# Performance work log

Measured on AMD Instinct MI355X. Metric: run time of the kernel, lower is better.

Reference implementation:

```python
import jax, jax.numpy as jnp
import numpy as np

B, N, C, H, W = 4, 5, 64, 96, 288
DOWNSAMPLE_RATE = 4
DISCRETE_RATIO = 0.4
DECAY_WEIGHTS = jax.nn.softmax(jnp.array([1.0, 0.5], dtype=jnp.float32))  # frame=1, decay=0.5


def _warp_one(img, theta):
    # img: (C,H,W), theta: (2,3). Matches F.affine_grid + F.grid_sample
    # (bilinear, zeros padding, align_corners=True).
    c, h, w = img.shape
    xs = jnp.linspace(-1.0, 1.0, w, dtype=img.dtype)
    ys = jnp.linspace(-1.0, 1.0, h, dtype=img.dtype)
    gy, gx = jnp.meshgrid(ys, xs, indexing='ij')
    base = jnp.stack([gx.ravel(), gy.ravel(), jnp.ones(h * w, img.dtype)], 0)  # (3, HW)
    g = theta @ base  # (2, HW) normalized coords
    px = (g[0] + 1.0) * 0.5 * (w - 1)
    py = (g[1] + 1.0) * 0.5 * (h - 1)
    x0 = jnp.floor(px); y0 = jnp.floor(py)
    wx = px - x0; wy = py - y0
    def tap(yy, xx):
        yi = jnp.clip(yy, 0, h - 1).astype(jnp.int32)
        xi = jnp.clip(xx, 0, w - 1).astype(jnp.int32)
        valid = ((yy >= 0) & (yy <= h - 1) & (xx >= 0) & (xx <= w - 1)).astype(img.dtype)
        return img[:, yi, xi] * valid  # (C, HW)
    out = (tap(y0, x0) * (1 - wx) * (1 - wy)
           + tap(y0, x0 + 1) * wx * (1 - wy)
           + tap(y0 + 1, x0) * (1 - wx) * wy
           + tap(y0 + 1, x0 + 1) * wx * wy)
    return out.reshape(c, h, w)


def _frame_score(hist, mlp_w, mlp_b):
    # hist: (B,N,C,H,W) -> per-pixel ego-vs-neighbor attention score (B,N,1,H,W).
    b, n, c, h, w = hist.shape
    node = hist.reshape(b, n, c, h * w).transpose(0, 3, 1, 2)  # (B, P, N, C)
    ego = node[:, :, 0]          # (B, P, C)
    neigh = node[:, :, 1:]       # (B, P, N-1, C)
    # Query rows are all the repeated ego vector -> one row suffices (identical math).
    s = jnp.einsum('bpc,bpkc->bpk', ego, neigh) / jnp.sqrt(jnp.asarray(c, hist.dtype))
    attn = jax.nn.softmax(s, axis=-1)
    ctx = jnp.einsum('bpk,bpkc->bpc', attn, neigh)
    sc = jax.nn.sigmoid(ctx @ mlp_w.T + mlp_b)                   # (B, P, 1)
    sc = jnp.broadcast_to(sc[:, :, None, :], (b, h * w, n - 1, 1))
    ego_sc = jnp.ones((b, h * w, 1, 1), hist.dtype)
    overall = jnp.concatenate([ego_sc, sc], axis=2)              # (B, P, N, 1)
    return overall.transpose(0, 2, 3, 1).reshape(b, n, 1, h, w)


def _forward(x0, x1, pairwise_t_matrix, mlp_w, mlp_b):
    x0g = x0.reshape(B, N, C, H, W)
    x1g = x1.reshape(B, N, C, H, W)

    # --- TemporalSampling: weighted per-frame scores, threshold, 3x3 max-pool ---
    conf = DECAY_WEIGHTS[0] * _frame_score(x0g, mlp_w, mlp_b) \
         + DECAY_WEIGHTS[1] * _frame_score(x1g, mlp_w, mlp_b)      # (B,N,1,H,W)
    mask = jnp.where(conf > 0.5, jnp.float32(1.0), jnp.float32(0.0))
    mask = jax.lax.reduce_window(mask, -jnp.inf, jax.lax.max,
                                 (1, 1, 1, 3, 3), (1, 1, 1, 1, 1), 'SAME')
    x = x0g * mask  # broadcast over C

    # --- normalize pairwise transform to 2x3 affine matrices ---
    t = pairwise_t_matrix[:, :, :, jnp.array([0, 1])][:, :, :, :, jnp.array([0, 1, 3])]  # (B,L,L,2,3)
    t = t.at[..., 0, 1].mul(H / W)
    t = t.at[..., 1, 0].mul(W / H)
    t = t.at[..., 0, 2].set(t[..., 0, 2] / (DOWNSAMPLE_RATE * DISCRETE_RATIO * W) * 2)
    t = t.at[..., 1, 2].set(t[..., 1, 2] / (DOWNSAMPLE_RATE * DISCRETE_RATIO * H) * 2)
    theta = t[:, 0]  # (B,N,2,3): warp each cav into ego frame

    # --- per-agent warp ---
    warped = jax.vmap(jax.vmap(_warp_one))(x, theta)  # (B,N,C,H,W)

    # --- AttenFusion: per-pixel NxN attention, keep ego row ---
    nf = warped.reshape(B, N, C, H * W).transpose(0, 3, 1, 2)  # (B, P, N, C)
    s = jnp.einsum('bpc,bpkc->bpk', nf[:, :, 0], nf) / jnp.sqrt(jnp.asarray(C, nf.dtype))
    attn = jax.nn.softmax(s, axis=-1)
    ctx = jnp.einsum('bpk,bpkc->bpc', attn, nf)                 # (B, P, C)
    x_fuse = ctx.transpose(0, 2, 1).reshape(B, C, H, W)
    return x_fuse


def setup_inputs() -> dict:
    key = jax.random.key(0)
    k0, k1, k2, k3 = jax.random.split(key, 4)
    x0 = jax.random.normal(k0, (B * N, C, H, W), dtype=jnp.float32)
    x1 = jax.random.normal(k1, (B * N, C, H, W), dtype=jnp.float32)
    eye = jnp.broadcast_to(jnp.eye(4, dtype=jnp.float32), (B, N, N, 4, 4))
    pairwise_t_matrix = eye + 0.01 * jax.random.normal(k2, (B, N, N, 4, 4), dtype=jnp.float32)
    mlp_w = 0.1 * jax.random.normal(k3, (1, C), dtype=jnp.float32)
    mlp_b = jnp.zeros((1,), dtype=jnp.float32)
    record_len = jnp.full((B,), N, dtype=jnp.int32)
    return {"x0": x0, "x1": x1, "pairwise_t_matrix": pairwise_t_matrix,
            "mlp_w": mlp_w, "mlp_b": mlp_b, "record_len": record_len}


def reference(x0, x1, pairwise_t_matrix, mlp_w, mlp_b, record_len):
    # record_len is uniform (=N) and only determines the static regrouping.
    return _forward(x0, x1, pairwise_t_matrix, mlp_w, mlp_b)
```

## Files before the change

### kernel.cpp

```cpp
#include <hip/hip_runtime.h>
#include <cmath>

#define BB 4
#define NN 5
#define CC 64
#define HH 96
#define WW 288
#define PP (HH*WW)
#define QP (PP/4)
#define BP (BB*PP)
#define BQ (BP/4)
#define TPITCH 65


static __device__ __forceinline__ float sigmoidf_(float x) {
    return 1.0f / (1.0f + expf(-x));
}
static __device__ __forceinline__ float4 f4zero() {
    return make_float4(0.f, 0.f, 0.f, 0.f);
}
static __device__ __forceinline__ void fma4s(float4& a, float s, const float4& v) {
    a.x += s * v.x; a.y += s * v.y; a.z += s * v.z; a.w += s * v.w;
}
static __device__ __forceinline__ void fma44(float4& a, const float4& s, const float4& v) {
    a.x += s.x * v.x; a.y += s.y * v.y; a.z += s.z * v.z; a.w += s.w * v.w;
}
static __device__ __forceinline__ float dot4(const float4& a, const float4& b) {
    return a.x*b.x + a.y*b.y + a.z*b.z + a.w*b.w;
}
static __device__ __forceinline__ float score4(const float* dd, const float* mm, float bias) {
    float s0 = dd[0]*0.125f, s1 = dd[1]*0.125f, s2 = dd[2]*0.125f, s3 = dd[3]*0.125f;
    float mx = fmaxf(fmaxf(s0, s1), fmaxf(s2, s3));
    float e0 = expf(s0-mx), e1 = expf(s1-mx), e2 = expf(s2-mx), e3 = expf(s3-mx);
    float inv = 1.0f / (e0+e1+e2+e3);
    float z = (e0*mm[0] + e1*mm[1] + e2*mm[2] + e3*mm[3]) * inv + bias;
    return sigmoidf_(z);
}

static __device__ __forceinline__ void theta_load(
    const float* __restrict__ pmat, int b, int n,
    float& t00, float& t01, float& t02, float& t10, float& t11, float& t12)
{
    const float* m = pmat + ((size_t)(b * NN + 0) * NN + n) * 16;
    t00 = m[0];
    t01 = m[1] * ((float)HH / (float)WW);
    t02 = m[3] * (float)(2.0 / (4.0 * 0.4 * (double)WW));
    t10 = m[4] * ((float)WW / (float)HH);
    t11 = m[5];
    t12 = m[7] * (float)(2.0 / (4.0 * 0.4 * (double)HH));
}

__global__ __launch_bounds__(256) void x1_part_kernel(
    const float4* __restrict__ x1, const float* __restrict__ mlp_w,
    float4* __restrict__ dpart1)
{
    int q   = blockIdx.x * 256 + threadIdx.x;
    int seg = blockIdx.y;
    int b  = q / QP;
    int qp = q - b * QP;
    const float4* base = x1 + (size_t)b * (NN*CC*QP) + qp;

    float4 d[4] = {f4zero(), f4zero(), f4zero(), f4zero()};
    float4 m[4] = {f4zero(), f4zero(), f4zero(), f4zero()};
    #pragma unroll 4
    for (int ci = 0; ci < 16; ci++) {
        int c = seg * 16 + ci;
        float4 e  = base[(size_t)c * QP];
        float  wc = mlp_w[c];
        #pragma unroll
        for (int k = 1; k < NN; k++) {
            float4 v = base[((size_t)k * CC + c) * QP];
            fma44(d[k-1], e, v);
            fma4s(m[k-1], wc, v);
        }
    }
    #pragma unroll
    for (int j = 0; j < 4; j++) {
        dpart1[((size_t)seg * 8 + j)     * BQ + q] = d[j];
        dpart1[((size_t)seg * 8 + 4 + j) * BQ + q] = m[j];
    }
}

__global__ __launch_bounds__(256) void transpose_mask_kernel(
    const float4* __restrict__ x0f4, const float* __restrict__ mlp_w,
    float4* __restrict__ x0t, float* __restrict__ dpx0)
{
    __shared__ float A[64 * TPITCH];
    __shared__ float Bsh[64 * TPITCH];
    __shared__ float redD[256];
    __shared__ float redM[256];
    __shared__ float wlds[64];

    int t   = threadIdx.x;
    int b   = blockIdx.y;
    int pt0 = blockIdx.x * 64;
    int c   = t >> 2, pq = t & 3;
    int pix = t >> 2, cg = t & 3;

    if (t < 64) wlds[t] = mlp_w[t];

    {
        const float4* src = x0f4 + ((size_t)(b*NN + 0) * CC + c) * QP
                                 + blockIdx.x * 16 + pq * 4;
        float4 r[4];
        #pragma unroll
        for (int j = 0; j < 4; j++) r[j] = src[j];
        #pragma unroll
        for (int j = 0; j < 4; j++) {
            int col = pq * 16 + j * 4;
            A[c*TPITCH + col+0] = r[j].x;
            A[c*TPITCH + col+1] = r[j].y;
            A[c*TPITCH + col+2] = r[j].z;
            A[c*TPITCH + col+3] = r[j].w;
        }
    }
    __syncthreads();
    float a[16];
    {
        #pragma unroll
        for (int j = 0; j < 16; j++) a[j] = A[(cg*16 + j)*TPITCH + pix];
        float4* dst = x0t + ((size_t)(b*NN + 0) * PP + pt0 + pix) * 16 + cg * 4;
        #pragma unroll
        for (int jj = 0; jj < 4; jj++)
            dst[jj] = make_float4(a[jj*4+0], a[jj*4+1], a[jj*4+2], a[jj*4+3]);
    }

    for (int k = 1; k < NN; k++) {
        const float4* src = x0f4 + ((size_t)(b*NN + k) * CC + c) * QP
                                 + blockIdx.x * 16 + pq * 4;
        float4 r[4];
        #pragma unroll
        for (int j = 0; j < 4; j++) r[j] = src[j];
        __syncthreads();
        #pragma unroll
        for (int j = 0; j < 4; j++) {
            int col = pq * 16 + j * 4;
            Bsh[c*TPITCH + col+0] = r[j].x;
            Bsh[c*TPITCH + col+1] = r[j].y;
            Bsh[c*TPITCH + col+2] = r[j].z;
            Bsh[c*TPITCH + col+3] = r[j].w;
        }
        __syncthreads();
        float bv[16];
        #pragma unroll
        for (int j = 0; j < 16; j++) bv[j] = Bsh[(cg*16 + j)*TPITCH + pix];
        float4* dst = x0t + ((size_t)(b*NN + k) * PP + pt0 + pix) * 16 + cg * 4;
        #pragma unroll
        for (int jj = 0; jj < 4; jj++)
            dst[jj] = make_float4(bv[jj*4+0], bv[jj*4+1], bv[jj*4+2], bv[jj*4+3]);

        float sd = 0.f, sm = 0.f;
        #pragma unroll
        for (int j = 0; j < 16; j++) {
            sd += a[j] * bv[j];
            sm += wlds[cg*16 + j] * bv[j];
        }
        redD[t] = sd;
        redM[t] = sm;
        __syncthreads();
        if (t < 64) {
            float dd = redD[t*4] + redD[t*4+1] + redD[t*4+2] + redD[t*4+3];
            float mm = redM[t*4] + redM[t*4+1] + redM[t*4+2] + redM[t*4+3];
            int gp = b * PP + pt0 + t;
            dpx0[(size_t)(k-1)   * BP + gp] = dd;
            dpx0[(size_t)(4+k-1) * BP + gp] = mm;
        }
    }
}

__global__ __launch_bounds__(256) void comb_kernel(
    const float4* __restrict__ dpart1, const float4* __restrict__ dpx0,
    const float* __restrict__ mlp_b, float4* __restrict__ premask)
{
    int q = blockIdx.x * 256 + threadIdx.x;
    float bias = mlp_b[0];

    float4 d1[8];
    #pragma unroll
    for (int j = 0; j < 8; j++) {
        float4 s = f4zero();
        #pragma unroll
        for (int seg = 0; seg < 4; seg++) {
            float4 v = dpart1[((size_t)seg * 8 + j) * BQ + q];
            s.x += v.x; s.y += v.y; s.z += v.z; s.w += v.w;
        }
        d1[j] = s;
    }
    float4 d0[8];
    #pragma unroll
    for (int j = 0; j < 8; j++) d0[j] = dpx0[(size_t)j * BQ + q];

    const float W0 = 0.6224593312018546f, W1 = 0.3775406687981454f;
    float4 res;
    #pragma unroll
    for (int kcomp = 0; kcomp < 4; kcomp++) {
        float dd0[4], mm0[4], dd1[4], mm1[4];
        #pragma unroll
        for (int j = 0; j < 4; j++) {
            dd0[j] = ((const float*)&d0[j])[kcomp];
            mm0[j] = ((const float*)&d0[4+j])[kcomp];
            dd1[j] = ((const float*)&d1[j])[kcomp];
            mm1[j] = ((const float*)&d1[4+j])[kcomp];
        }
        float sc0 = score4(dd0, mm0, bias);
        float sc1 = score4(dd1, mm1, bias);
        float conf = W0 * sc0 + W1 * sc1;
        ((float*)&res)[kcomp] = (conf > 0.5f) ? 1.f : 0.f;
    }
    premask[q] = res;
}

__global__ __launch_bounds__(256) void pool_kernel(
    const float* __restrict__ pre, float4* __restrict__ pooled)
{
    int q  = blockIdx.x * 256 + threadIdx.x;
    int b  = q / QP;
    int qp = q - b * QP;
    int p0 = qp * 4;
    int h  = p0 / WW;
    int w0 = p0 - h * WW;
    const float* pb = pre + (size_t)b * PP;
    float m[4] = {0.f, 0.f, 0.f, 0.f};
    #pragma unroll
    for (int dy = -1; dy <= 1; dy++) {
        int y = h + dy;
        if (y < 0 || y >= HH) continue;
        const float* row = pb + y * WW;
        float c_[6];
        float4 mid = *(const float4*)(row + w0);
        c_[0] = (w0 > 0) ? row[w0 - 1] : 0.f;
        c_[1] = mid.x; c_[2] = mid.y; c_[3] = mid.z; c_[4] = mid.w;
        c_[5] = (w0 + 4 < WW) ? row[w0 + 4] : 0.f;
        #pragma unroll
        for (int j = 0; j < 4; j++)
            m[j] = fmaxf(m[j], fmaxf(c_[j], fmaxf(c_[j+1], c_[j+2])));
    }
    pooled[q] = make_float4(m[0], m[1], m[2], m[3]);
}

__global__ __launch_bounds__(256) void fuse_kernel(
    const float4* __restrict__ x0t, const float* __restrict__ pmat,
    const float* __restrict__ pooled, float* __restrict__ out)
{
    int g   = blockIdx.x * 256 + threadIdx.x;
    int pix = g >> 4;
    int cq  = g & 15;
    int b = pix / PP;
    int p = pix - b * PP;
    int h = p / WW;
    int w = p - h * WW;

    float gx = -1.0f + 2.0f * (float)w / (float)(WW - 1);
    float gy = -1.0f + 2.0f * (float)h / (float)(HH - 1);
    const float* poolb = pooled + (size_t)b * PP;

    float4 wv[NN];
    #pragma unroll
    for (int n = 0; n < NN; n++) {
        float t00, t01, t02, t10, t11, t12;
        theta_load(pmat, b, n, t00, t01, t02, t10, t11, t12);
        float g0 = t00 * gx + t01 * gy + t02;
        float g1 = t10 * gx + t11 * gy + t12;
        float fx = (g0 + 1.0f) * 0.5f * (float)(WW - 1);
        float fy = (g1 + 1.0f) * 0.5f * (float)(HH - 1);
        float x0f = floorf(fx), y0f = floorf(fy);
        float wx = fx - x0f, wy = fy - y0f;
        float bw[4] = { (1.f - wx) * (1.f - wy), wx * (1.f - wy),
                        (1.f - wx) * wy,         wx * wy };
        const float4* fr = x0t + (size_t)(b * NN + n) * PP * 16;
        float4 acc = f4zero();
        #pragma unroll
        for (int t = 0; t < 4; t++) {
            float xx = (t & 1) ? (x0f + 1.0f) : x0f;
            float yy = (t >> 1) ? (y0f + 1.0f) : y0f;
            int xi = min(max((int)xx, 0), WW - 1);
            int yi = min(max((int)yy, 0), HH - 1);
            float valid = (yy >= 0.0f && yy <= (float)(HH - 1) &&
                           xx >= 0.0f && xx <= (float)(WW - 1)) ? 1.0f : 0.0f;
            int off = yi * WW + xi;
            float mk = (n == 0) ? 1.0f : poolb[off];
            float wgt = bw[t] * valid * mk;
            float4 v = fr[(size_t)off * 16 + cq];
            fma4s(acc, wgt, v);
        }
        wv[n] = acc;
    }

    float dt[NN];
    #pragma unroll
    for (int n = 0; n < NN; n++) dt[n] = dot4(wv[0], wv[n]);
    #pragma unroll
    for (int n = 0; n < NN; n++) {
        #pragma unroll
        for (int msk = 1; msk < 16; msk <<= 1)
            dt[n] += __shfl_xor(dt[n], msk, 16);
    }

    float s[NN], attn[NN];
    float mx = -INFINITY;
    #pragma unroll
    for (int n = 0; n < NN; n++) { s[n] = dt[n] * 0.125f; mx = fmaxf(mx, s[n]); }
    float sum = 0.f;
    #pragma unroll
    for (int n = 0; n < NN; n++) { attn[n] = expf(s[n] - mx); sum += attn[n]; }
    float inv = 1.0f / sum;

    float4 o = f4zero();
    #pragma unroll
    for (int n = 0; n < NN; n++) fma4s(o, attn[n] * inv, wv[n]);

    size_t ob = ((size_t)(b * CC + cq * 4)) * PP + p;
    out[ob]                = o.x;
    out[ob + (size_t)PP]   = o.y;
    out[ob + (size_t)2*PP] = o.z;
    out[ob + (size_t)3*PP] = o.w;
}

extern "C" void kernel_launch(void* const* d_in, const int* in_sizes, int n_in,
                              void* d_out, int out_size, void* d_ws, size_t ws_size,
                              hipStream_t stream) {
    float*       x0    = (float*)d_in[0];
    float*       x1    = (float*)d_in[1];
    const float* pmat  = (const float*)d_in[2];
    const float* mlp_w = (const float*)d_in[3];
    const float* mlp_b = (const float*)d_in[4];
    float* out = (float*)d_out;

    float4* x0f4    = (float4*)x0;
    float4* x1f4    = (float4*)x1;
    float4* out4    = (float4*)out;
    float4* dpart1  = out4;
    float*  dpx0_f  = out + (size_t)128 * BQ;
    float4* dpx0_4  = (float4*)dpx0_f;
    float4* x0t     = x1f4;
    float*  pre_f   = x0;
    float4* pre_4   = x0f4;
    float*  pool_f  = x0 + (size_t)BP;
    float4* pool_4  = (float4*)pool_f;

    dim3 blk(256);
    x1_part_kernel       <<<dim3(BQ/256, 4),  blk, 0, stream>>>(x1f4, mlp_w, dpart1);
    transpose_mask_kernel<<<dim3(PP/64, BB),  blk, 0, stream>>>(x0f4, mlp_w, x0t, dpx0_f);
    comb_kernel          <<<dim3(BQ/256),     blk, 0, stream>>>(dpart1, dpx0_4, mlp_b, pre_4);
    pool_kernel          <<<dim3(BQ/256),     blk, 0, stream>>>(pre_f, pool_4);
    fuse_kernel          <<<dim3(BP/16),      blk, 0, stream>>>(x0t, pmat, pool_f, out);
}
```

Baseline: 388.6 us.

## Fuse x1 attention-score computation into transpose kernel and drop partial sums

Removes the separate x1_part_kernel, which computed per-segment partial dot products over x1 and wrote 32 partial planes. The transpose kernel now also loads x1 through the shared-memory tile and computes the full ego-neighbour dots and MLP projections directly. This eliminates one launch, the partial-sum write and reread, and the 4-way reduction in comb_kernel. The transposed x0 buffer moves to workspace when it is large enough. The cost is that the transpose kernel does twice the serial work per block, with more syncthreads on the x1 path.

```diff
diff --git a/kernel.cpp b/kernel.cpp
--- a/kernel.cpp
+++ b/kernel.cpp
@@ -22,9 +22,6 @@
 static __device__ __forceinline__ void fma4s(float4& a, float s, const float4& v) {
     a.x += s * v.x; a.y += s * v.y; a.z += s * v.z; a.w += s * v.w;
 }
-static __device__ __forceinline__ void fma44(float4& a, const float4& s, const float4& v) {
-    a.x += s.x * v.x; a.y += s.y * v.y; a.z += s.z * v.z; a.w += s.w * v.w;
-}
 static __device__ __forceinline__ float dot4(const float4& a, const float4& b) {
     return a.x*b.x + a.y*b.y + a.z*b.z + a.w*b.w;
 }
@@ -50,43 +47,12 @@
     t12 = m[7] * (float)(2.0 / (4.0 * 0.4 * (double)HH));
 }
 
-__global__ __launch_bounds__(256) void x1_part_kernel(
-    const float4* __restrict__ x1, const float* __restrict__ mlp_w,
-    float4* __restrict__ dpart1)
-{
-    int q   = blockIdx.x * 256 + threadIdx.x;
-    int seg = blockIdx.y;
-    int b  = q / QP;
-    int qp = q - b * QP;
-    const float4* base = x1 + (size_t)b * (NN*CC*QP) + qp;
-
-    float4 d[4] = {f4zero(), f4zero(), f4zero(), f4zero()};
-    float4 m[4] = {f4zero(), f4zero(), f4zero(), f4zero()};
-    #pragma unroll 4
-    for (int ci = 0; ci < 16; ci++) {
-        int c = seg * 16 + ci;
-        float4 e  = base[(size_t)c * QP];
-        float  wc = mlp_w[c];
-        #pragma unroll
-        for (int k = 1; k < NN; k++) {
-            float4 v = base[((size_t)k * CC + c) * QP];
-            fma44(d[k-1], e, v);
-            fma4s(m[k-1], wc, v);
-        }
-    }
-    #pragma unroll
-    for (int j = 0; j < 4; j++) {
-        dpart1[((size_t)seg * 8 + j)     * BQ + q] = d[j];
-        dpart1[((size_t)seg * 8 + 4 + j) * BQ + q] = m[j];
-    }
-}
-
 __global__ __launch_bounds__(256) void transpose_mask_kernel(
-    const float4* __restrict__ x0f4, const float* __restrict__ mlp_w,
-    float4* __restrict__ x0t, float* __restrict__ dpx0)
-{
-    __shared__ float A[64 * TPITCH];
-    __shared__ float Bsh[64 * TPITCH];
+    const float4* __restrict__ x0f4, const float4* __restrict__ x1f4,
+    const float* __restrict__ mlp_w, float4* __restrict__ x0t,
+    float* __restrict__ dd_out)
+{
+    __shared__ float T[64 * TPITCH];
     __shared__ float redD[256];
     __shared__ float redM[256];
     __shared__ float wlds[64];
@@ -99,113 +65,94 @@
 
     if (t < 64) wlds[t] = mlp_w[t];
 
-    {
-        const float4* src = x0f4 + ((size_t)(b*NN + 0) * CC + c) * QP
-                                 + blockIdx.x * 16 + pq * 4;
-        float4 r[4];
-        #pragma unroll
-        for (int j = 0; j < 4; j++) r[j] = src[j];
-        #pragma unroll
-        for (int j = 0; j < 4; j++) {
-            int col = pq * 16 + j * 4;
-            A[c*TPITCH + col+0] = r[j].x;
-            A[c*TPITCH + col+1] = r[j].y;
-            A[c*TPITCH + col+2] = r[j].z;
-            A[c*TPITCH + col+3] = r[j].w;
+    float a0[16], a1[16];
+
+    #pragma unroll
+    for (int srcs = 0; srcs < 2; srcs++) {
+        const float4* xs = srcs ? x1f4 : x0f4;
+        float* aref = srcs ? a1 : a0;
+        for (int k = 0; k < NN; k++) {
+            const float4* src = xs + ((size_t)(b*NN + k) * CC + c) * QP
+                                   + blockIdx.x * 16 + pq * 4;
+            float4 r[4];
+            #pragma unroll
+            for (int j = 0; j < 4; j++) r[j] = src[j];
+            __syncthreads();
+            #pragma unroll
+            for (int j = 0; j < 4; j++) {
+                int col = pq * 16 + j * 4;
+                T[c*TPITCH + col+0] = r[j].x;
+                T[c*TPITCH + col+1] = r[j].y;
+                T[c*TPITCH + col+2] = r[j].z;
+                T[c*TPITCH + col+3] = r[j].w;
+            }
+            __syncthreads();
+            float bv[16];
+            #pragma unroll
+            for (int j = 0; j < 16; j++) bv[j] = T[(cg*16 + j)*TPITCH + pix];
+
+            if (srcs == 0) {
+                float4* dst = x0t + ((size_t)(b*NN + k) * PP + pt0 + pix) * 16 + cg * 4;
+                #pragma unroll
+                for (int jj = 0; jj < 4; jj++)
+                    dst[jj] = make_float4(bv[jj*4+0], bv[jj*4+1], bv[jj*4+2], bv[jj*4+3]);
+            }
+
+            if (k == 0) {
+                #pragma unroll
+                for (int j = 0; j < 16; j++) aref[j] = bv[j];
+            } else {
+                float sd = 0.f, sm = 0.f;
+                #pragma unroll
+                for (int j = 0; j < 16; j++) {
+                    sd += aref[j] * bv[j];
+                    sm += wlds[cg*16 + j] * bv[j];
+                }
+                redD[t] = sd;
+                redM[t] = sm;
+                __syncthreads();
+                if (t < 64) {
+                    float dd = redD[t*4] + redD[t*4+1] + redD[t*4+2] + redD[t*4+3];
+                    float mm = redM[t*4] + redM[t*4+1] + redM[t*4+2] + redM[t*4+3];
+                    int gp = b * PP + pt0 + t;
+                    dd_out[(size_t)(srcs*8 + (k-1))     * BP + gp] = dd;
+                    dd_out[(size_t)(srcs*8 + 4 + (k-1)) * BP + gp] = mm;
+                }
+            }
         }
     }
-    __syncthreads();
-    float a[16];
-    {
-        #pragma unroll
-        for (int j = 0; j < 16; j++) a[j] = A[(cg*16 + j)*TPITCH + pix];
-        float4* dst = x0t + ((size_t)(b*NN + 0) * PP + pt0 + pix) * 16 + cg * 4;
-        #pragma unroll
-        for (int jj = 0; jj < 4; jj++)
-            dst[jj] = make_float4(a[jj*4+0], a[jj*4+1], a[jj*4+2], a[jj*4+3]);
-    }
-
-    for (int k = 1; k < NN; k++) {
-        const float4* src = x0f4 + ((size_t)(b*NN + k) * CC + c) * QP
-                                 + blockIdx.x * 16 + pq * 4;
-        float4 r[4];
-        #pragma unroll
-        for (int j = 0; j < 4; j++) r[j] = src[j];
-        __syncthreads();
-        #pragma unroll
-        for (int j = 0; j < 4; j++) {
-            int col = pq * 16 + j * 4;
-            Bsh[c*TPITCH + col+0] = r[j].x;
-            Bsh[c*TPITCH + col+1] = r[j].y;
-            Bsh[c*TPITCH + col+2] = r[j].z;
-            Bsh[c*TPITCH + col+3] = r[j].w;
-        }
-        __syncthreads();
-        float bv[16];
-        #pragma unroll
-        for (int j = 0; j < 16; j++) bv[j] = Bsh[(cg*16 + j)*TPITCH + pix];
-        float4* dst = x0t + ((size_t)(b*NN + k) * PP + pt0 + pix) * 16 + cg * 4;
-        #pragma unroll
-        for (int jj = 0; jj < 4; jj++)
-            dst[jj] = make_float4(bv[jj*4+0], bv[jj*4+1], bv[jj*4+2], bv[jj*4+3]);
-
-        float sd = 0.f, sm = 0.f;
-        #pragma unroll
-        for (int j = 0; j < 16; j++) {
-            sd += a[j] * bv[j];
-            sm += wlds[cg*16 + j] * bv[j];
-        }
-        redD[t] = sd;
-        redM[t] = sm;
-        __syncthreads();
-        if (t < 64) {
-            float dd = redD[t*4] + redD[t*4+1] + redD[t*4+2] + redD[t*4+3];
-            float mm = redM[t*4] + redM[t*4+1] + redM[t*4+2] + redM[t*4+3];
-            int gp = b * PP + pt0 + t;
-            dpx0[(size_t)(k-1)   * BP + gp] = dd;
-            dpx0[(size_t)(4+k-1) * BP + gp] = mm;
-        }
-    }
 }
 
 __global__ __launch_bounds__(256) void comb_kernel(
-    const float4* __restrict__ dpart1, const float4* __restrict__ dpx0,
-    const float* __restrict__ mlp_b, float4* __restrict__ premask)
+    const float4* __restrict__ dd, const float* __restrict__ mlp_b,
+    float4* __restrict__ premask)
 {
     int q = blockIdx.x * 256 + threadIdx.x;
     float bias = mlp_b[0];
 
-    float4 d1[8];
+    float4 v0[8], v1[8];
     #pragma unroll
     for (int j = 0; j < 8; j++) {
-        float4 s = f4zero();
-        #pragma unroll
-        for (int seg = 0; seg < 4; seg++) {
-            float4 v = dpart1[((size_t)seg * 8 + j) * BQ + q];
-            s.x += v.x; s.y += v.y; s.z += v.z; s.w += v.w;
-        }
-        d1[j] = s;
-    }
-    float4 d0[8];
-    #pragma unroll
-    for (int j = 0; j < 8; j++) d0[j] = dpx0[(size_t)j * BQ + q];
+        v0[j] = dd[(size_t)j       * BQ + q];
+        v1[j] = dd[(size_t)(8 + j) * BQ + q];
+    }
 
     const float W0 = 0.6224593312018546f, W1 = 0.3775406687981454f;
     float4 res;
     #pragma unroll
-    for (int kcomp = 0; kcomp < 4; kcomp++) {
+    for (int kc = 0; kc < 4; kc++) {
         float dd0[4], mm0[4], dd1[4], mm1[4];
         #pragma unroll
         for (int j = 0; j < 4; j++) {
-            dd0[j] = ((const float*)&d0[j])[kcomp];
-            mm0[j] = ((const float*)&d0[4+j])[kcomp];
-            dd1[j] = ((const float*)&d1[j])[kcomp];
-            mm1[j] = ((const float*)&d1[4+j])[kcomp];
+            dd0[j] = ((const float*)&v0[j])[kc];
+            mm0[j] = ((const float*)&v0[4+j])[kc];
+            dd1[j] = ((const float*)&v1[j])[kc];
+            mm1[j] = ((const float*)&v1[4+j])[kc];
         }
         float sc0 = score4(dd0, mm0, bias);
         float sc1 = score4(dd1, mm1, bias);
         float conf = W0 * sc0 + W1 * sc1;
-        ((float*)&res)[kcomp] = (conf > 0.5f) ? 1.f : 0.f;
+        ((float*)&res)[kc] = (conf > 0.5f) ? 1.f : 0.f;
     }
     premask[q] = res;
 }
@@ -326,22 +273,27 @@
     const float* mlp_b = (const float*)d_in[4];
     float* out = (float*)d_out;
 
-    float4* x0f4    = (float4*)x0;
-    float4* x1f4    = (float4*)x1;
-    float4* out4    = (float4*)out;
-    float4* dpart1  = out4;
-    float*  dpx0_f  = out + (size_t)128 * BQ;
-    float4* dpx0_4  = (float4*)dpx0_f;
-    float4* x0t     = x1f4;
-    float*  pre_f   = x0;
-    float4* pre_4   = x0f4;
-    float*  pool_f  = x0 + (size_t)BP;
-    float4* pool_4  = (float4*)pool_f;
+    const size_t x0t_bytes = (size_t)NN * CC * PP * sizeof(float);
+    float4* x0t;
+    if (ws_size >= x0t_bytes && d_ws != nullptr) {
+        x0t = (float4*)d_ws;
+    } else {
+        x0t = (float4*)x1;
+    }
+
+    float4* x0f4   = (float4*)x0;
+    float4* x1f4   = (float4*)x1;
+    float4* out4   = (float4*)out;
+    float*  dd_f   = out;
+    float4* dd_4   = out4;
+    float*  pre_f  = x1;
+    float4* pre_4  = x1f4;
+    float*  pool_f = x1 + (size_t)BP;
+    float4* pool_4 = (float4*)pool_f;
 
     dim3 blk(256);
-    x1_part_kernel       <<<dim3(BQ/256, 4),  blk, 0, stream>>>(x1f4, mlp_w, dpart1);
-    transpose_mask_kernel<<<dim3(PP/64, BB),  blk, 0, stream>>>(x0f4, mlp_w, x0t, dpx0_f);
-    comb_kernel          <<<dim3(BQ/256),     blk, 0, stream>>>(dpart1, dpx0_4, mlp_b, pre_4);
-    pool_kernel          <<<dim3(BQ/256),     blk, 0, stream>>>(pre_f, pool_4);
-    fuse_kernel          <<<dim3(BP/16),      blk, 0, stream>>>(x0t, pmat, pool_f, out);
-}
+    transpose_mask_kernel<<<dim3(PP/64, BB), blk, 0, stream>>>(x0f4, x1f4, mlp_w, x0t, dd_f);
+    comb_kernel          <<<dim3(BQ/256),    blk, 0, stream>>>(dd_4, mlp_b, pre_4);
+    pool_kernel          <<<dim3(BQ/256),    blk, 0, stream>>>(pre_f, pool_4);
+    fuse_kernel          <<<dim3(BP/16),     blk, 0, stream>>>(x0t, pmat, pool_f, out);
+}
```

After: 401.0 us. 3.2% more time.
